# Kernel optimization log

Measured on AMD Instinct MI355X. Metric: run time of the kernel, lower is better.

Reference implementation:

```python
import jax, jax.numpy as jnp
import numpy as np


def gcn_conv(x, row, col, ew, W, b, N):
    # GCNConv: add self-loops (weight 1), symmetric normalization, X @ W, scatter-add, + bias
    loop = jnp.arange(N, dtype=row.dtype)
    r = jnp.concatenate([row, loop])
    c = jnp.concatenate([col, loop])
    w = jnp.concatenate([ew, jnp.ones((N,), dtype=x.dtype)])
    deg = jax.ops.segment_sum(w, c, num_segments=N)
    dinv = jnp.where(deg > 0, jax.lax.rsqrt(deg), 0.0).astype(x.dtype)
    norm = dinv[r] * w * dinv[c]                  # [E+N]
    h = x @ W                                     # [N, out]
    msg = h[r] * norm[:, None]                    # gather + scale
    out = jax.ops.segment_sum(msg, c, num_segments=N)  # scatter-add to targets
    return out + b


def setup_inputs() -> dict:
    key = jax.random.key(0)
    ks = jax.random.split(key, 10)
    N, E, C_in, C_hid, C_out = 65536, 1048576, 16, 64, 2
    x = jax.random.normal(ks[0], (N, C_in), dtype=jnp.float32)
    edge_index = jax.random.randint(ks[1], (2, E), 0, N, dtype=jnp.int64)
    edge_weight = jax.random.uniform(ks[2], (E,), dtype=jnp.float32)
    s = lambda k, sh, fan: jax.random.normal(k, sh, dtype=jnp.float32) / np.sqrt(fan)
    return {
        "x": x,
        "edge_index": edge_index,
        "edge_weight": edge_weight,
        "W1": s(ks[3], (C_in, C_hid), C_in),
        "b1": jnp.zeros((C_hid,), dtype=jnp.float32),
        "W2": s(ks[4], (C_hid, C_hid), C_hid),
        "b2": jnp.zeros((C_hid,), dtype=jnp.float32),
        "Wl": s(ks[5], (C_hid, C_out), C_hid),
        "bl": jnp.zeros((C_out,), dtype=jnp.float32),
    }


def reference(x, edge_index, edge_weight, W1, b1, W2, b2, Wl, bl):
    N = x.shape[0]
    row, col = edge_index[0], edge_index[1]  # source -> target
    h = jax.nn.relu(gcn_conv(x, row, col, edge_weight, W1, b1, N))
    h = jax.nn.relu(gcn_conv(h, row, col, edge_weight, W2, b2, N))
    return h @ Wl + bl
```

## Files before the change

### kernel.cpp

```cpp
#include <hip/hip_runtime.h>

#define NSB 1024
#define NBUCK(n) ((n) >> 8)

__global__ __launch_bounds__(256) void s1_hist(const int* __restrict__ col,
                                               int* __restrict__ F, int E, int chunk) {
    __shared__ int cnt[256];
    int t = threadIdx.x, b = blockIdx.x;
    cnt[t] = 0;
    __syncthreads();
    int s = b * chunk, e = min(E, s + chunk);
    for (int i = s + t; i < e; i += 256) atomicAdd(&cnt[col[i] >> 8], 1);
    __syncthreads();
    F[t * NSB + b] = cnt[t];
}

__global__ void scanF1(int* __restrict__ F, int* __restrict__ bsum, int n) {
    __shared__ int sd[256];
    int t = threadIdx.x, i = blockIdx.x * 256 + t;
    int v = (i < n) ? F[i] : 0;
    sd[t] = v;
    __syncthreads();
    for (int o = 1; o < 256; o <<= 1) {
        int x = (t >= o) ? sd[t - o] : 0;
        __syncthreads();
        sd[t] += x;
        __syncthreads();
    }
    if (i < n) F[i] = sd[t] - v;
    if (t == 255) bsum[blockIdx.x] = sd[255];
}

__global__ void scanF2(const int* __restrict__ bsum, int* __restrict__ boff, int nb) {
    __shared__ int sd[1024];
    int t = threadIdx.x;
    int v = (t < nb) ? bsum[t] : 0;
    sd[t] = v;
    __syncthreads();
    for (int o = 1; o < 1024; o <<= 1) {
        int x = (t >= o) ? sd[t - o] : 0;
        __syncthreads();
        sd[t] += x;
        __syncthreads();
    }
    if (t < nb) boff[t] = sd[t] - v;
}

__global__ void scanF3(int* __restrict__ F, const int* __restrict__ boff, int n) {
    int i = blockIdx.x * blockDim.x + threadIdx.x;
    if (i < n) F[i] += boff[i >> 8];
}

__global__ __launch_bounds__(256) void s3_scatter(const int* __restrict__ col,
                                                  const int* __restrict__ row,
                                                  const float* __restrict__ ew,
                                                  const int* __restrict__ F,
                                                  int2* __restrict__ tmp, int E, int chunk) {
    __shared__ int off[256];
    __shared__ int cur[256];
    int t = threadIdx.x, b = blockIdx.x;
    off[t] = F[t * NSB + b];
    cur[t] = 0;
    __syncthreads();
    int s = b * chunk, e = min(E, s + chunk);
    for (int i = s + t; i < e; i += 256) {
        int c = col[i];
        int bk = c >> 8;
        int rk = atomicAdd(&cur[bk], 1);
        tmp[off[bk] + rk] = make_int2(row[i] | ((c & 255) << 16), __float_as_int(ew[i]));
    }
}

__global__ __launch_bounds__(256) void s4_fine(const int2* __restrict__ tmp,
                                               const int* __restrict__ F,
                                               int2* __restrict__ pack,
                                               float* __restrict__ dinv,
                                               int* __restrict__ start,
                                               const float* __restrict__ x,
                                               const float* __restrict__ W1,
                                               float* __restrict__ g1,
                                               int n, int E, int nbuck) {
    __shared__ int   fcnt[256];
    __shared__ float fdeg[256];
    __shared__ int   foff[256];
    __shared__ int   fcur[256];
    __shared__ float Ws[16 * 64];
    int t = threadIdx.x, b = blockIdx.x;
    reinterpret_cast<float4*>(Ws)[t] = reinterpret_cast<const float4*>(W1)[t];
    fcnt[t] = 0; fdeg[t] = 0.f; fcur[t] = 0;
    __syncthreads();
    int segS = F[b * NSB];
    int segE = (b == nbuck - 1) ? E : F[(b + 1) * NSB];
    for (int i = segS + t; i < segE; i += 256) {
        int2 v = tmp[i];
        int f = (v.x >> 16) & 255;
        atomicAdd(&fcnt[f], 1);
        atomicAdd(&fdeg[f], __int_as_float(v.y));
    }
    __syncthreads();
    int val = fcnt[t];
    foff[t] = val;
    __syncthreads();
    for (int o = 1; o < 256; o <<= 1) {
        int xk = (t >= o) ? foff[t - o] : 0;
        __syncthreads();
        foff[t] += xk;
        __syncthreads();
    }
    int excl = foff[t] - val;
    int c = (b << 8) | t;
    float di = rsqrtf(fdeg[t] + 1.0f);
    if (c < n) {
        dinv[c]  = di;
        start[c] = segS + excl;
    }
    if (b == nbuck - 1 && t == 255) start[n] = E;
    __syncthreads();
    foff[t] = excl;
    __syncthreads();
    for (int i = segS + t; i < segE; i += 256) {
        int2 v = tmp[i];
        int f = (v.x >> 16) & 255;
        int rk = atomicAdd(&fcur[f], 1);
        pack[segS + foff[f] + rk] = make_int2(v.x & 0xFFFF, v.y);
    }
    if (c >= n) return;
    float xv[16];
    const float4* xr = reinterpret_cast<const float4*>(x + (size_t)c * 16);
#pragma unroll
    for (int i = 0; i < 4; ++i)
        *reinterpret_cast<float4*>(&xv[i * 4]) = xr[i];
    float4* orow = reinterpret_cast<float4*>(g1 + ((size_t)c << 6));
    for (int jb = 0; jb < 16; ++jb) {
        float4 acc = make_float4(0.f, 0.f, 0.f, 0.f);
#pragma unroll
        for (int k = 0; k < 16; ++k) {
            float hk = xv[k];
            const float4 wv = *reinterpret_cast<const float4*>(&Ws[k * 64 + jb * 4]);
            acc.x += hk * wv.x; acc.y += hk * wv.y;
            acc.z += hk * wv.z; acc.w += hk * wv.w;
        }
        acc.x *= di; acc.y *= di; acc.z *= di; acc.w *= di;
        orow[jb] = acc;
    }
}

__global__ __launch_bounds__(256) void gemm_hid(const float* __restrict__ h,
                                                const float* __restrict__ W,
                                                const float* __restrict__ dinv,
                                                float* __restrict__ out, int n) {
    __shared__ float Ws[64 * 64];
    int t = threadIdx.x;
#pragma unroll
    for (int i = 0; i < 16; ++i) Ws[i * 256 + t] = W[i * 256 + t];
    __syncthreads();
    int node = blockIdx.x * 256 + t;
    if (node >= n) return;
    float hv[64];
    const float4* hr = reinterpret_cast<const float4*>(h + ((size_t)node << 6));
#pragma unroll
    for (int i = 0; i < 16; ++i)
        *reinterpret_cast<float4*>(&hv[i * 4]) = hr[i];
    float di = dinv[node];
    float4* orow = reinterpret_cast<float4*>(out + ((size_t)node << 6));
    for (int jb = 0; jb < 16; ++jb) {
        float4 acc = make_float4(0.f, 0.f, 0.f, 0.f);
#pragma unroll
        for (int k = 0; k < 64; ++k) {
            float hk = hv[k];
            const float4 wv = *reinterpret_cast<const float4*>(&Ws[k * 64 + jb * 4]);
            acc.x += hk * wv.x; acc.y += hk * wv.y;
            acc.z += hk * wv.z; acc.w += hk * wv.w;
        }
        acc.x *= di; acc.y *= di; acc.z *= di; acc.w *= di;
        orow[jb] = acc;
    }
}

__device__ __forceinline__ float4 gather_acc(const int* __restrict__ start,
                                             const int2* __restrict__ pack,
                                             const float* __restrict__ g,
                                             int wid, int sub, int ch4) {
    int s = start[wid], e = start[wid + 1];
    float4 acc = make_float4(0.f, 0.f, 0.f, 0.f);
    int i = s;
    for (; i + 7 < e; i += 8) {
        int2 pa = pack[i + sub];
        int2 pb = pack[i + 4 + sub];
        float wa = __int_as_float(pa.y), wb = __int_as_float(pb.y);
        const float4 va = *reinterpret_cast<const float4*>(g + ((size_t)pa.x << 6) + ch4);
        const float4 vb = *reinterpret_cast<const float4*>(g + ((size_t)pb.x << 6) + ch4);
        acc.x += va.x * wa; acc.y += va.y * wa; acc.z += va.z * wa; acc.w += va.w * wa;
        acc.x += vb.x * wb; acc.y += vb.y * wb; acc.z += vb.z * wb; acc.w += vb.w * wb;
    }
    if (i + 3 < e) {
        int2 pa = pack[i + sub];
        float wa = __int_as_float(pa.y);
        const float4 va = *reinterpret_cast<const float4*>(g + ((size_t)pa.x << 6) + ch4);
        acc.x += va.x * wa; acc.y += va.y * wa; acc.z += va.z * wa; acc.w += va.w * wa;
        i += 4;
    }
    int rem = e - i;
    if (sub < rem) {
        int2 pa = pack[i + sub];
        float wa = __int_as_float(pa.y);
        const float4 va = *reinterpret_cast<const float4*>(g + ((size_t)pa.x << 6) + ch4);
        acc.x += va.x * wa; acc.y += va.y * wa; acc.z += va.z * wa; acc.w += va.w * wa;
    }
#pragma unroll
    for (int m = 16; m <= 32; m <<= 1) {
        acc.x += __shfl_xor(acc.x, m, 64);
        acc.y += __shfl_xor(acc.y, m, 64);
        acc.z += __shfl_xor(acc.z, m, 64);
        acc.w += __shfl_xor(acc.w, m, 64);
    }
    return acc;
}

__global__ __launch_bounds__(256) void gather_mid(const int* __restrict__ start,
                                                  const int2* __restrict__ pack,
                                                  const float* __restrict__ g,
                                                  const float* __restrict__ dinv,
                                                  const float* __restrict__ b,
                                                  float* __restrict__ out, int n) {
    int wid = (blockIdx.x * blockDim.x + threadIdx.x) >> 6;
    if (wid >= n) return;
    int lane = threadIdx.x & 63;
    int sub = lane >> 4;
    int ch4 = (lane & 15) << 2;
    float4 acc = gather_acc(start, pack, g, wid, sub, ch4);
    if (sub == 0) {
        float di = dinv[wid];
        const float4 g0 = *reinterpret_cast<const float4*>(g + ((size_t)wid << 6) + ch4);
        const float4 bb = *reinterpret_cast<const float4*>(b + ch4);
        float4 r;
        r.x = fmaxf(di * (acc.x + g0.x) + bb.x, 0.f);
        r.y = fmaxf(di * (acc.y + g0.y) + bb.y, 0.f);
        r.z = fmaxf(di * (acc.z + g0.z) + bb.z, 0.f);
        r.w = fmaxf(di * (acc.w + g0.w) + bb.w, 0.f);
        *reinterpret_cast<float4*>(out + ((size_t)wid << 6) + ch4) = r;
    }
}

__global__ __launch_bounds__(256) void gather_head(const int* __restrict__ start,
                                                   const int2* __restrict__ pack,
                                                   const float* __restrict__ g,
                                                   const float* __restrict__ dinv,
                                                   const float* __restrict__ b,
                                                   const float* __restrict__ Wl,
                                                   const float* __restrict__ bl,
                                                   float* __restrict__ out, int n) {
    int wid = (blockIdx.x * blockDim.x + threadIdx.x) >> 6;
    if (wid >= n) return;
    int lane = threadIdx.x & 63;
    int sub = lane >> 4;
    int ch4 = (lane & 15) << 2;
    float4 acc = gather_acc(start, pack, g, wid, sub, ch4);
    if (sub == 0) {
        float di = dinv[wid];
        const float4 g0 = *reinterpret_cast<const float4*>(g + ((size_t)wid << 6) + ch4);
        const float4 bb = *reinterpret_cast<const float4*>(b + ch4);
        float4 h;
        h.x = fmaxf(di * (acc.x + g0.x) + bb.x, 0.f);
        h.y = fmaxf(di * (acc.y + g0.y) + bb.y, 0.f);
        h.z = fmaxf(di * (acc.z + g0.z) + bb.z, 0.f);
        h.w = fmaxf(di * (acc.w + g0.w) + bb.w, 0.f);
        float s0 = h.x * Wl[(ch4 + 0) * 2] + h.y * Wl[(ch4 + 1) * 2] +
                   h.z * Wl[(ch4 + 2) * 2] + h.w * Wl[(ch4 + 3) * 2];
        float s1 = h.x * Wl[(ch4 + 0) * 2 + 1] + h.y * Wl[(ch4 + 1) * 2 + 1] +
                   h.z * Wl[(ch4 + 2) * 2 + 1] + h.w * Wl[(ch4 + 3) * 2 + 1];
#pragma unroll
        for (int m = 1; m <= 8; m <<= 1) {
            s0 += __shfl_xor(s0, m, 64);
            s1 += __shfl_xor(s1, m, 64);
        }
        if (lane == 0) {
            out[(size_t)wid * 2 + 0] = s0 + bl[0];
            out[(size_t)wid * 2 + 1] = s1 + bl[1];
        }
    }
}

extern "C" void kernel_launch(void* const* d_in, const int* in_sizes, int n_in,
                              void* d_out, int out_size, void* d_ws, size_t ws_size,
                              hipStream_t stream) {
    const float* x  = (const float*)d_in[0];
    const int*   ei = (const int*)d_in[1];
    const float* ew = (const float*)d_in[2];
    const float* W1 = (const float*)d_in[3];
    const float* b1 = (const float*)d_in[4];
    const float* W2 = (const float*)d_in[5];
    const float* b2 = (const float*)d_in[6];
    const float* Wl = (const float*)d_in[7];
    const float* bl = (const float*)d_in[8];
    float* out = (float*)d_out;

    const int N = in_sizes[0] / 16;
    const int E = in_sizes[2];
    const int* row = ei;
    const int* col = ei + E;
    const int NB    = (N + 255) / 256;
    const int nbuck = N >> 8;
    const int chunk = (E + NSB - 1) / NSB;
    const int FSZ   = nbuck * NSB;
    const int FB    = (FSZ + 255) / 256;

    char* p = (char*)d_ws;
    int2*  pack = (int2*)p;   p += (size_t)E * 8;
    float* bufA = (float*)p;  p += (size_t)N * 64 * 4;
    char*  r2   = p;          p += (size_t)N * 64 * 4;
    float* dinv = (float*)p;  p += (size_t)N * 4;
    int* startO = (int*)p;    p += (size_t)(N + 1) * 4;

    int2* tmp  = (int2*)r2;
    int*  F    = (int*)(r2 + (size_t)E * 8);
    int*  bsum = F + FSZ;
    int*  boff = bsum + FB;
    float* bufB = (float*)r2;

    s1_hist<<<NSB, 256, 0, stream>>>(col, F, E, chunk);
    scanF1<<<FB, 256, 0, stream>>>(F, bsum, FSZ);
    scanF2<<<1, 1024, 0, stream>>>(bsum, boff, FB);
    scanF3<<<FB, 256, 0, stream>>>(F, boff, FSZ);
    s3_scatter<<<NSB, 256, 0, stream>>>(col, row, ew, F, tmp, E, chunk);
    s4_fine<<<nbuck, 256, 0, stream>>>(tmp, F, pack, dinv, startO, x, W1, bufA, N, E, nbuck);

    gather_mid<<<(N + 3) / 4, 256, 0, stream>>>(startO, pack, bufA, dinv, b1, bufB, N);

    gemm_hid<<<NB, 256, 0, stream>>>(bufB, W2, dinv, bufA, N);

    gather_head<<<(N + 3) / 4, 256, 0, stream>>>(startO, pack, bufA, dinv, b2, Wl, bl, out, N);
}
```

Before: 156.5 us.

## Store transformed features and edge weights in fp16 to halve gather traffic

The per-node transformed features (g1 and the layer-2 GEMM output) are now stored as fp16, and the CSR pack entry shrinks from int2 to a 32-bit word holding a 16-bit local source index and an fp16 edge weight. The gather kernels convert back to fp32 and accumulate in fp32. This is meant to cut the memory traffic of the random-access neighbour gathers and the edge stream. In exchange it loses precision, and the 16-bit source index depends on the bucket encoding already used (row values below 65536), so it only works for N up to 65536.

```diff
diff --git a/kernel.cpp b/kernel.cpp
--- a/kernel.cpp
+++ b/kernel.cpp
@@ -1,7 +1,12 @@
 #include <hip/hip_runtime.h>
+#include <hip/hip_fp16.h>
 
 #define NSB 1024
-#define NBUCK(n) ((n) >> 8)
+
+__device__ __forceinline__ unsigned pack_h2(float a, float b) {
+    __half2 h = __floats2half2_rn(a, b);
+    return *reinterpret_cast<unsigned*>(&h);
+}
 
 __global__ __launch_bounds__(256) void s1_hist(const int* __restrict__ col,
                                                int* __restrict__ F, int E, int chunk) {
@@ -73,12 +78,12 @@
 
 __global__ __launch_bounds__(256) void s4_fine(const int2* __restrict__ tmp,
                                                const int* __restrict__ F,
-                                               int2* __restrict__ pack,
+                                               unsigned* __restrict__ pack,
                                                float* __restrict__ dinv,
                                                int* __restrict__ start,
                                                const float* __restrict__ x,
                                                const float* __restrict__ W1,
-                                               float* __restrict__ g1,
+                                               __half* __restrict__ g1,
                                                int n, int E, int nbuck) {
     __shared__ int   fcnt[256];
     __shared__ float fdeg[256];
@@ -122,7 +127,9 @@
         int2 v = tmp[i];
         int f = (v.x >> 16) & 255;
         int rk = atomicAdd(&fcur[f], 1);
-        pack[segS + foff[f] + rk] = make_int2(v.x & 0xFFFF, v.y);
+        __half hw = __float2half_rn(__int_as_float(v.y));
+        pack[segS + foff[f] + rk] =
+            (unsigned)(v.x & 0xFFFF) | ((unsigned)*reinterpret_cast<unsigned short*>(&hw) << 16);
     }
     if (c >= n) return;
     float xv[16];
@@ -130,7 +137,7 @@
 #pragma unroll
     for (int i = 0; i < 4; ++i)
         *reinterpret_cast<float4*>(&xv[i * 4]) = xr[i];
-    float4* orow = reinterpret_cast<float4*>(g1 + ((size_t)c << 6));
+    uint2* orow = reinterpret_cast<uint2*>(g1 + ((size_t)c << 6));
     for (int jb = 0; jb < 16; ++jb) {
         float4 acc = make_float4(0.f, 0.f, 0.f, 0.f);
 #pragma unroll
@@ -140,15 +147,17 @@
             acc.x += hk * wv.x; acc.y += hk * wv.y;
             acc.z += hk * wv.z; acc.w += hk * wv.w;
         }
-        acc.x *= di; acc.y *= di; acc.z *= di; acc.w *= di;
-        orow[jb] = acc;
+        uint2 st;
+        st.x = pack_h2(acc.x * di, acc.y * di);
+        st.y = pack_h2(acc.z * di, acc.w * di);
+        orow[jb] = st;
     }
 }
 
 __global__ __launch_bounds__(256) void gemm_hid(const float* __restrict__ h,
                                                 const float* __restrict__ W,
                                                 const float* __restrict__ dinv,
-                                                float* __restrict__ out, int n) {
+                                                __half* __restrict__ out, int n) {
     __shared__ float Ws[64 * 64];
     int t = threadIdx.x;
 #pragma unroll
@@ -162,7 +171,7 @@
     for (int i = 0; i < 16; ++i)
         *reinterpret_cast<float4*>(&hv[i * 4]) = hr[i];
     float di = dinv[node];
-    float4* orow = reinterpret_cast<float4*>(out + ((size_t)node << 6));
+    uint2* orow = reinterpret_cast<uint2*>(out + ((size_t)node << 6));
     for (int jb = 0; jb < 16; ++jb) {
         float4 acc = make_float4(0.f, 0.f, 0.f, 0.f);
 #pragma unroll
@@ -172,39 +181,51 @@
             acc.x += hk * wv.x; acc.y += hk * wv.y;
             acc.z += hk * wv.z; acc.w += hk * wv.w;
         }
-        acc.x *= di; acc.y *= di; acc.z *= di; acc.w *= di;
-        orow[jb] = acc;
-    }
+        uint2 st;
+        st.x = pack_h2(acc.x * di, acc.y * di);
+        st.y = pack_h2(acc.z * di, acc.w * di);
+        orow[jb] = st;
+    }
+}
+
+__device__ __forceinline__ float4 load_row4(const __half* __restrict__ g,
+                                            unsigned pk, int ch4, float* wout) {
+    unsigned short hw = (unsigned short)(pk >> 16);
+    *wout = __half2float(*reinterpret_cast<__half*>(&hw));
+    uint2 u = *reinterpret_cast<const uint2*>(g + ((size_t)(pk & 0xFFFFu) << 6) + ch4);
+    float2 a = __half22float2(*reinterpret_cast<__half2*>(&u.x));
+    float2 b = __half22float2(*reinterpret_cast<__half2*>(&u.y));
+    return make_float4(a.x, a.y, b.x, b.y);
 }
 
 __device__ __forceinline__ float4 gather_acc(const int* __restrict__ start,
-                                             const int2* __restrict__ pack,
-                                             const float* __restrict__ g,
+                                             const unsigned* __restrict__ pack,
+                                             const __half* __restrict__ g,
                                              int wid, int sub, int ch4) {
     int s = start[wid], e = start[wid + 1];
     float4 acc = make_float4(0.f, 0.f, 0.f, 0.f);
     int i = s;
     for (; i + 7 < e; i += 8) {
-        int2 pa = pack[i + sub];
-        int2 pb = pack[i + 4 + sub];
-        float wa = __int_as_float(pa.y), wb = __int_as_float(pb.y);
-        const float4 va = *reinterpret_cast<const float4*>(g + ((size_t)pa.x << 6) + ch4);
-        const float4 vb = *reinterpret_cast<const float4*>(g + ((size_t)pb.x << 6) + ch4);
+        unsigned pa = pack[i + sub];
+        unsigned pb = pack[i + 4 + sub];
+        float wa, wb;
+        float4 va = load_row4(g, pa, ch4, &wa);
+        float4 vb = load_row4(g, pb, ch4, &wb);
         acc.x += va.x * wa; acc.y += va.y * wa; acc.z += va.z * wa; acc.w += va.w * wa;
         acc.x += vb.x * wb; acc.y += vb.y * wb; acc.z += vb.z * wb; acc.w += vb.w * wb;
     }
     if (i + 3 < e) {
-        int2 pa = pack[i + sub];
-        float wa = __int_as_float(pa.y);
-        const float4 va = *reinterpret_cast<const float4*>(g + ((size_t)pa.x << 6) + ch4);
+        unsigned pa = pack[i + sub];
+        float wa;
+        float4 va = load_row4(g, pa, ch4, &wa);
         acc.x += va.x * wa; acc.y += va.y * wa; acc.z += va.z * wa; acc.w += va.w * wa;
         i += 4;
     }
     int rem = e - i;
     if (sub < rem) {
-        int2 pa = pack[i + sub];
-        float wa = __int_as_float(pa.y);
-        const float4 va = *reinterpret_cast<const float4*>(g + ((size_t)pa.x << 6) + ch4);
+        unsigned pa = pack[i + sub];
+        float wa;
+        float4 va = load_row4(g, pa, ch4, &wa);
         acc.x += va.x * wa; acc.y += va.y * wa; acc.z += va.z * wa; acc.w += va.w * wa;
     }
 #pragma unroll
@@ -218,8 +239,8 @@
 }
 
 __global__ __launch_bounds__(256) void gather_mid(const int* __restrict__ start,
-                                                  const int2* __restrict__ pack,
-                                                  const float* __restrict__ g,
+                                                  const unsigned* __restrict__ pack,
+                                                  const __half* __restrict__ g,
                                                   const float* __restrict__ dinv,
                                                   const float* __restrict__ b,
                                                   float* __restrict__ out, int n) {
@@ -231,20 +252,22 @@
     float4 acc = gather_acc(start, pack, g, wid, sub, ch4);
     if (sub == 0) {
         float di = dinv[wid];
-        const float4 g0 = *reinterpret_cast<const float4*>(g + ((size_t)wid << 6) + ch4);
+        uint2 u0 = *reinterpret_cast<const uint2*>(g + ((size_t)wid << 6) + ch4);
+        float2 ga = __half22float2(*reinterpret_cast<__half2*>(&u0.x));
+        float2 gb = __half22float2(*reinterpret_cast<__half2*>(&u0.y));
         const float4 bb = *reinterpret_cast<const float4*>(b + ch4);
         float4 r;
-        r.x = fmaxf(di * (acc.x + g0.x) + bb.x, 0.f);
-        r.y = fmaxf(di * (acc.y + g0.y) + bb.y, 0.f);
-        r.z = fmaxf(di * (acc.z + g0.z) + bb.z, 0.f);
-        r.w = fmaxf(di * (acc.w + g0.w) + bb.w, 0.f);
+        r.x = fmaxf(di * (acc.x + ga.x) + bb.x, 0.f);
+        r.y = fmaxf(di * (acc.y + ga.y) + bb.y, 0.f);
+        r.z = fmaxf(di * (acc.z + gb.x) + bb.z, 0.f);
+        r.w = fmaxf(di * (acc.w + gb.y) + bb.w, 0.f);
         *reinterpret_cast<float4*>(out + ((size_t)wid << 6) + ch4) = r;
     }
 }
 
 __global__ __launch_bounds__(256) void gather_head(const int* __restrict__ start,
-                                                   const int2* __restrict__ pack,
-                                                   const float* __restrict__ g,
+                                                   const unsigned* __restrict__ pack,
+                                                   const __half* __restrict__ g,
                                                    const float* __restrict__ dinv,
                                                    const float* __restrict__ b,
                                                    const float* __restrict__ Wl,
@@ -258,13 +281,15 @@
     float4 acc = gather_acc(start, pack, g, wid, sub, ch4);
     if (sub == 0) {
         float di = dinv[wid];
-        const float4 g0 = *reinterpret_cast<const float4*>(g + ((size_t)wid << 6) + ch4);
+        uint2 u0 = *reinterpret_cast<const uint2*>(g + ((size_t)wid << 6) + ch4);
+        float2 ga = __half22float2(*reinterpret_cast<__half2*>(&u0.x));
+        float2 gb = __half22float2(*reinterpret_cast<__half2*>(&u0.y));
         const float4 bb = *reinterpret_cast<const float4*>(b + ch4);
         float4 h;
-        h.x = fmaxf(di * (acc.x + g0.x) + bb.x, 0.f);
-        h.y = fmaxf(di * (acc.y + g0.y) + bb.y, 0.f);
-        h.z = fmaxf(di * (acc.z + g0.z) + bb.z, 0.f);
-        h.w = fmaxf(di * (acc.w + g0.w) + bb.w, 0.f);
+        h.x = fmaxf(di * (acc.x + ga.x) + bb.x, 0.f);
+        h.y = fmaxf(di * (acc.y + ga.y) + bb.y, 0.f);
+        h.z = fmaxf(di * (acc.z + gb.x) + bb.z, 0.f);
+        h.w = fmaxf(di * (acc.w + gb.y) + bb.w, 0.f);
         float s0 = h.x * Wl[(ch4 + 0) * 2] + h.y * Wl[(ch4 + 1) * 2] +
                    h.z * Wl[(ch4 + 2) * 2] + h.w * Wl[(ch4 + 3) * 2];
         float s1 = h.x * Wl[(ch4 + 0) * 2 + 1] + h.y * Wl[(ch4 + 1) * 2 + 1] +
@@ -306,11 +331,11 @@
     const int FB    = (FSZ + 255) / 256;
 
     char* p = (char*)d_ws;
-    int2*  pack = (int2*)p;   p += (size_t)E * 8;
-    float* bufA = (float*)p;  p += (size_t)N * 64 * 4;
-    char*  r2   = p;          p += (size_t)N * 64 * 4;
-    float* dinv = (float*)p;  p += (size_t)N * 4;
-    int* startO = (int*)p;    p += (size_t)(N + 1) * 4;
+    unsigned* pack = (unsigned*)p;  p += (size_t)E * 4;
+    __half*   bufA = (__half*)p;    p += (size_t)N * 64 * 2;
+    char*     r2   = p;             p += (size_t)N * 64 * 4;
+    float*    dinv = (float*)p;     p += (size_t)N * 4;
+    int*    startO = (int*)p;       p += (size_t)(N + 1) * 4;
 
     int2* tmp  = (int2*)r2;
     int*  F    = (int*)(r2 + (size_t)E * 8);
```

New measurement: 138.7 us. -11.4%, faster.
